# Optimization experiments

Measured on AMD Instinct MI355X. Metric: run time of the kernel, lower is better.

The kernel has to match this reference:

```python
import jax, jax.numpy as jnp
import numpy as np

B, SD, VD, AD, E, K = 32768, 96, 512, 12, 8, 2
EPS_LN = 1e-5

def _ln(x, g, b):
    m = x.mean(-1, keepdims=True)
    v = ((x - m) ** 2).mean(-1, keepdims=True)
    return (x - m) / jnp.sqrt(v + EPS_LN) * g + b

def setup_inputs() -> dict:
    key = jax.random.key(0)
    ks = iter(jax.random.split(key, 64))
    def w(shape, s=0.02):
        return jax.random.normal(next(ks), shape, dtype=jnp.float32) * s
    inp = {
        'state_obs': jax.random.normal(next(ks), (B, SD), dtype=jnp.float32),
        'vlm_feature': jax.random.normal(next(ks), (B, VD), dtype=jnp.float32),
        # state encoder (per-expert stacked): 96->256->128, Linear+ELU+LN each
        'sw1': w((E, SD, 256)), 'sb1': jnp.zeros((E, 256)), 'sg1': jnp.ones((E, 256)), 'sh1': jnp.zeros((E, 256)),
        'sw2': w((E, 256, 128)), 'sb2': jnp.zeros((E, 128)), 'sg2': jnp.ones((E, 128)), 'sh2': jnp.zeros((E, 128)),
        # vlm encoder: 512->512->256
        'vw1': w((E, VD, 512)), 'vb1': jnp.zeros((E, 512)), 'vg1': jnp.ones((E, 512)), 'vh1': jnp.zeros((E, 512)),
        'vw2': w((E, 512, 256)), 'vb2': jnp.zeros((E, 256)), 'vg2': jnp.ones((E, 256)), 'vh2': jnp.zeros((E, 256)),
        # fusion: (128+256)=384 -> 512 -> 256 -> 12 (act+LN except last)
        'fw1': w((E, 384, 512)), 'fb1': jnp.zeros((E, 512)), 'fg1': jnp.ones((E, 512)), 'fh1': jnp.zeros((E, 512)),
        'fw2': w((E, 512, 256)), 'fb2': jnp.zeros((E, 256)), 'fg2': jnp.ones((E, 256)), 'fh2': jnp.zeros((E, 256)),
        'fw3': w((E, 256, AD)), 'fb3': jnp.zeros((E, AD)),
        # gate: (96+512)=608 -> 256 -> 128 -> 8, act between hidden layers only
        'gw1': w((SD + VD, 256)), 'gb1': jnp.zeros((256,)),
        'gw2': w((256, 128)), 'gb2': jnp.zeros((128,)),
        'gw3': w((128, E)), 'gb3': jnp.zeros((E,)),
        'logstd': jnp.full((AD,), -1.0, dtype=jnp.float32),
    }
    return inp

def reference(state_obs, vlm_feature,
              sw1, sb1, sg1, sh1, sw2, sb2, sg2, sh2,
              vw1, vb1, vg1, vh1, vw2, vb2, vg2, vh2,
              fw1, fb1, fg1, fh1, fw2, fb2, fg2, fh2, fw3, fb3,
              gw1, gb1, gw2, gb2, gw3, gb3, logstd):
    act = jax.nn.elu
    # run ALL experts densely (faithful to the module)
    h = _ln(act(jnp.einsum('bi,eio->beo', state_obs, sw1) + sb1), sg1, sh1)   # [B,E,256]
    obs_feat = _ln(act(jnp.einsum('bei,eio->beo', h, sw2) + sb2), sg2, sh2)   # [B,E,128]
    h = _ln(act(jnp.einsum('bi,eio->beo', vlm_feature, vw1) + vb1), vg1, vh1) # [B,E,512]
    vlm_feat = _ln(act(jnp.einsum('bei,eio->beo', h, vw2) + vb2), vg2, vh2)   # [B,E,256]
    fused = jnp.concatenate([obs_feat, vlm_feat], axis=-1)                     # [B,E,384]
    h = _ln(act(jnp.einsum('bei,eio->beo', fused, fw1) + fb1), fg1, fh1)
    h = _ln(act(jnp.einsum('bei,eio->beo', h, fw2) + fb2), fg2, fh2)
    all_outputs = jnp.einsum('bei,eio->beo', h, fw3) + fb3                     # [B,E,AD]
    # gate
    g = jnp.concatenate([state_obs, vlm_feature], axis=-1)
    g = act(g @ gw1 + gb1)
    g = act(g @ gw2 + gb2)
    gate_logits = g @ gw3 + gb3
    gate_probs = jax.nn.softmax(gate_logits, axis=-1)                          # [B,E]
    top_k_scores, top_k_indices = jax.lax.top_k(gate_probs, K)                 # [B,K]
    selected = jnp.take_along_axis(all_outputs, top_k_indices[:, :, None], axis=1)  # [B,K,AD]
    weights = top_k_scores / (top_k_scores.sum(axis=1, keepdims=True) + 1e-9)
    fused_output = (selected * weights[:, :, None]).sum(axis=1)                # [B,AD]
    # auxiliary load-balancing loss (Switch-style)
    dispatch = jax.nn.one_hot(top_k_indices, E, dtype=gate_probs.dtype).sum(1) # [B,E]
    f = dispatch.mean(0) / K
    P = gate_probs.mean(0)
    aux_loss = E * jnp.sum(f * P)
    action = fused_output  # deterministic path
    return action, aux_loss, top_k_indices, top_k_scores
```

## Files before the change

kernel.cpp:

```cpp
#include <hip/hip_runtime.h>
#include <cstdint>
#include <cstddef>

#define BROWS 32768
#define NEXP 8
#define CAP 10240
#define CAPBLK (CAP / 64)

typedef short bf16x8 __attribute__((ext_vector_type(8)));
typedef float f32x4 __attribute__((ext_vector_type(4)));
typedef float f32x2 __attribute__((ext_vector_type(2)));

__device__ __forceinline__ unsigned short f2b(float f) {
  union { float f; unsigned u; } v; v.f = f;
  unsigned r = (v.u + 0x7fffu + ((v.u >> 16) & 1u)) >> 16;
  return (unsigned short)r;
}
__device__ __forceinline__ float b2f(unsigned short s) {
  union { unsigned u; float f; } v; v.u = ((unsigned)s) << 16; return v.f;
}
__device__ __forceinline__ float fast_elu(float x) {
  return x > 0.f ? x : __expf(x) - 1.f;
}


__global__ void k_convert_pad(const float* __restrict__ src, unsigned short* __restrict__ dst,
                              int rows, int sc, int dc) {
  int i = blockIdx.x * 256 + threadIdx.x;
  if (i >= rows * dc) return;
  int r = i / dc, c = i % dc;
  float v = (c < sc) ? src[(size_t)r * sc + c] : 0.f;
  dst[i] = f2b(v);
}

__global__ void k_wtrans(const float* __restrict__ src, unsigned short* __restrict__ dst,
                         int K, int N, int Kpad) {
  __shared__ float tile[32][33];
  int e = blockIdx.z;
  int k0 = blockIdx.x * 32, n0 = blockIdx.y * 32;
  int tx = threadIdx.x, ty = threadIdx.y;
  for (int i = 0; i < 32; i += 8) {
    int k = k0 + ty + i;
    tile[ty + i][tx] = (k < K) ? src[((size_t)e * K + k) * N + n0 + tx] : 0.f;
  }
  __syncthreads();
  for (int i = 0; i < 32; i += 8) {
    int n = n0 + ty + i;
    dst[((size_t)e * N + n) * Kpad + k0 + tx] = f2b(tile[tx][ty + i]);
  }
}

__global__ void k_zero(int* p, int n) {
  int i = blockIdx.x * 64 + threadIdx.x;
  if (i < n) p[i] = 0;
}

template<bool TWOSRC>
__launch_bounds__(256, 4)
__global__ void k_gemm32(const float* __restrict__ A0, int As0,
                         const float* __restrict__ A1, int As1, int Ks,
                         const float* __restrict__ W, const float* __restrict__ bias,
                         int K, int N, float* __restrict__ Out) {
  __shared__ float At[32][132];
  __shared__ float Bs[32][132];

  int tid = threadIdx.x;
  int rb = blockIdx.x * 128, nb = blockIdx.y * 128;
  int tx = tid & 15, tyg = tid >> 4;
  int arow = tid >> 1, aq = (tid & 1) * 16;
  int brow = tid >> 3, bc = (tid & 7) * 16;

  f32x2 acc[8][4] = {};

  float4 a0, a1, a2, a3, b0, b1, b2, b3;
  {
    const float* arp = (!TWOSRC || aq < Ks)
        ? (A0 + (size_t)(rb + arow) * As0 + aq)
        : (A1 + (size_t)(rb + arow) * As1 + (aq - Ks));
    a0 = *(const float4*)(arp);
    a1 = *(const float4*)(arp + 4);
    a2 = *(const float4*)(arp + 8);
    a3 = *(const float4*)(arp + 12);
    const float* brp = W + (size_t)brow * N + nb + bc;
    b0 = *(const float4*)(brp);
    b1 = *(const float4*)(brp + 4);
    b2 = *(const float4*)(brp + 8);
    b3 = *(const float4*)(brp + 12);
  }

  const int NT = K / 32;
  for (int kt = 0; kt < NT; ++kt) {
    __syncthreads();
    At[aq + 0][arow] = a0.x;  At[aq + 1][arow] = a0.y;
    At[aq + 2][arow] = a0.z;  At[aq + 3][arow] = a0.w;
    At[aq + 4][arow] = a1.x;  At[aq + 5][arow] = a1.y;
    At[aq + 6][arow] = a1.z;  At[aq + 7][arow] = a1.w;
    At[aq + 8][arow] = a2.x;  At[aq + 9][arow] = a2.y;
    At[aq + 10][arow] = a2.z; At[aq + 11][arow] = a2.w;
    At[aq + 12][arow] = a3.x; At[aq + 13][arow] = a3.y;
    At[aq + 14][arow] = a3.z; At[aq + 15][arow] = a3.w;
    *(float4*)(&Bs[brow][bc])      = b0;
    *(float4*)(&Bs[brow][bc + 4])  = b1;
    *(float4*)(&Bs[brow][bc + 8])  = b2;
    *(float4*)(&Bs[brow][bc + 12]) = b3;
    __syncthreads();

    if (kt + 1 < NT) {
      int ka = (kt + 1) * 32 + aq;
      const float* arp = (!TWOSRC || ka < Ks)
          ? (A0 + (size_t)(rb + arow) * As0 + ka)
          : (A1 + (size_t)(rb + arow) * As1 + (ka - Ks));
      a0 = *(const float4*)(arp);
      a1 = *(const float4*)(arp + 4);
      a2 = *(const float4*)(arp + 8);
      a3 = *(const float4*)(arp + 12);
      const float* brp = W + (size_t)((kt + 1) * 32 + brow) * N + nb + bc;
      b0 = *(const float4*)(brp);
      b1 = *(const float4*)(brp + 4);
      b2 = *(const float4*)(brp + 8);
      b3 = *(const float4*)(brp + 12);
    }

#pragma unroll 4
    for (int kk = 0; kk < 32; ++kk) {
      float4 av0 = *(const float4*)(&At[kk][tyg * 8]);
      float4 av1 = *(const float4*)(&At[kk][tyg * 8 + 4]);
      float4 bq0 = *(const float4*)(&Bs[kk][tx * 8]);
      float4 bq1 = *(const float4*)(&Bs[kk][tx * 8 + 4]);
      f32x2 bp0 = {bq0.x, bq0.y}, bp1 = {bq0.z, bq0.w};
      f32x2 bp2 = {bq1.x, bq1.y}, bp3 = {bq1.z, bq1.w};
      float av[8] = {av0.x, av0.y, av0.z, av0.w, av1.x, av1.y, av1.z, av1.w};
#pragma unroll
      for (int i = 0; i < 8; ++i) {
        f32x2 as = {av[i], av[i]};
        acc[i][0] = __builtin_elementwise_fma(as, bp0, acc[i][0]);
        acc[i][1] = __builtin_elementwise_fma(as, bp1, acc[i][1]);
        acc[i][2] = __builtin_elementwise_fma(as, bp2, acc[i][2]);
        acc[i][3] = __builtin_elementwise_fma(as, bp3, acc[i][3]);
      }
    }
  }

  float4 bia0 = *(const float4*)(&bias[nb + tx * 8]);
  float4 bia1 = *(const float4*)(&bias[nb + tx * 8 + 4]);
  float bia[8] = {bia0.x, bia0.y, bia0.z, bia0.w, bia1.x, bia1.y, bia1.z, bia1.w};

#pragma unroll
  for (int i = 0; i < 8; ++i) {
    float o[8];
#pragma unroll
    for (int j = 0; j < 4; ++j) {
      o[2 * j]     = acc[i][j][0] + bia[2 * j];
      o[2 * j + 1] = acc[i][j][1] + bia[2 * j + 1];
    }
#pragma unroll
    for (int j = 0; j < 8; ++j) o[j] = (o[j] > 0.f) ? o[j] : expm1f(o[j]);
    size_t orow = (size_t)(rb + tyg * 8 + i) * N + nb + tx * 8;
    float4 w0; w0.x = o[0]; w0.y = o[1]; w0.z = o[2]; w0.w = o[3];
    float4 w1; w1.x = o[4]; w1.y = o[5]; w1.z = o[6]; w1.w = o[7];
    *(float4*)(&Out[orow]) = w0;
    *(float4*)(&Out[orow + 4]) = w1;
  }
}

#define ACTION_SZ (32768 * 12)
#define AUX_OFF   ACTION_SZ
#define IDX_OFF   (ACTION_SZ + 1)
#define SCO_OFF   (ACTION_SZ + 1 + 32768 * 2)

__global__ void k_gatetop(const float* __restrict__ gh2,
                          const float* __restrict__ gw3, const float* __restrict__ gb3,
                          float* __restrict__ out, float* __restrict__ aux,
                          int* __restrict__ bcnt, float* __restrict__ selbuf) {
  int tid = threadIdx.x;
  int b = blockIdx.x * 256 + tid;
  int lane = tid & 63, w = tid >> 6;
  __shared__ float sprob[8];
  if (tid < 8) sprob[tid] = 0.f;
  __syncthreads();

  float lg[8];
#pragma unroll
  for (int j = 0; j < 8; ++j) lg[j] = gb3[j];
  for (int k = 0; k < 128; ++k) {
    float h = gh2[(size_t)b * 128 + k];
#pragma unroll
    for (int j = 0; j < 8; ++j) lg[j] += h * gw3[k * 8 + j];
  }
  float m = lg[0];
#pragma unroll
  for (int j = 1; j < 8; ++j) m = fmaxf(m, lg[j]);
  float probs[8], sum = 0.f;
#pragma unroll
  for (int j = 0; j < 8; ++j) { float p = expf(lg[j] - m); probs[j] = p; sum += p; }
  float inv = 1.f / sum;
#pragma unroll
  for (int j = 0; j < 8; ++j) probs[j] *= inv;
  int i0 = 0, i1;
  float v0 = -1e30f;
#pragma unroll
  for (int j = 0; j < 8; ++j) if (probs[j] > v0) { v0 = probs[j]; i0 = j; }
  float v1 = -1e30f; i1 = (i0 == 0) ? 1 : 0;
#pragma unroll
  for (int j = 0; j < 8; ++j) if (j != i0 && probs[j] > v1) { v1 = probs[j]; i1 = j; }
  float wsum = v0 + v1 + 1e-9f;
  float w0 = v0 / wsum, w1 = v1 / wsum;

  out[IDX_OFF + (size_t)b * 2 + 0] = (float)i0;
  out[IDX_OFF + (size_t)b * 2 + 1] = (float)i1;
  out[SCO_OFF + (size_t)b * 2 + 0] = v0;
  out[SCO_OFF + (size_t)b * 2 + 1] = v1;
  selbuf[(size_t)b * 4 + 0] = (float)i0;
  selbuf[(size_t)b * 4 + 1] = (float)i1;
  selbuf[(size_t)b * 4 + 2] = w0;
  selbuf[(size_t)b * 4 + 3] = w1;

#pragma unroll
  for (int e2 = 0; e2 < 8; ++e2) {
    unsigned long long mm = __ballot(i0 == e2) | __ballot(i1 == e2);
    if (lane == 0) bcnt[(blockIdx.x * 4 + w) * 8 + e2] = __popcll(mm);
  }

#pragma unroll
  for (int j = 0; j < 8; ++j) {
    float p = probs[j];
#pragma unroll
    for (int mk = 1; mk <= 32; mk <<= 1) p += __shfl_xor(p, mk, 64);
    if (lane == 0) atomicAdd(&sprob[j], p);
  }
  __syncthreads();
  if (tid < 8) atomicAdd(&aux[tid], sprob[tid]);
}

__global__ void k_scan(const int* __restrict__ bcnt, int* __restrict__ bbase,
                       int* __restrict__ cnt) {
  __shared__ int psum[8][8];
  int tid = threadIdx.x;
  int e2 = tid & 7, seg = tid >> 3;
  int s = 0;
  for (int i = 0; i < 64; ++i) s += bcnt[(seg * 64 + i) * 8 + e2];
  psum[seg][e2] = s;
  __syncthreads();
  int base = 0;
  for (int t = 0; t < seg; ++t) base += psum[t][e2];
  int run = base;
  for (int i = 0; i < 64; ++i) {
    bbase[(seg * 64 + i) * 8 + e2] = run;
    run += bcnt[(seg * 64 + i) * 8 + e2];
  }
  if (seg == 7) cnt[e2] = run;
}

__global__ void k_fill(const float* __restrict__ selbuf, const int* __restrict__ bbase,
                       int* __restrict__ perm) {
  int gidx = blockIdx.x;
  int lane = threadIdx.x;
  int b = gidx * 64 + lane;
  int i0 = (int)selbuf[(size_t)b * 4 + 0];
  int i1 = (int)selbuf[(size_t)b * 4 + 1];
  unsigned long long lt = (1ull << lane) - 1ull;
#pragma unroll
  for (int e2 = 0; e2 < 8; ++e2) {
    unsigned long long mm = __ballot(i0 == e2) | __ballot(i1 == e2);
    if (i0 == e2 || i1 == e2) {
      int s = bbase[gidx * 8 + e2] + (int)__popcll(mm & lt);
      if (s < CAP) perm[e2 * CAP + s] = b;
    }
  }
}

__global__ void k_auxfinal(const int* __restrict__ cnt, const float* __restrict__ aux,
                           float* __restrict__ out) {
  if (threadIdx.x == 0) {
    float s = 0.f;
#pragma unroll
    for (int e = 0; e < 8; ++e) {
      float f = (float)cnt[e] / (32768.f * 2.f);
      float P = aux[e] / 32768.f;
      s += f * P;
    }
    out[AUX_OFF] = 8.f * s;
  }
}

template<int K1, int N1, int N2, bool GATHER, bool FCHAIN>
__launch_bounds__(512, 4)
__global__ void k_chain(const unsigned short* __restrict__ A, int As,
                        const int* __restrict__ perm, const int* __restrict__ cnt,
                        const unsigned short* __restrict__ W1, const float* __restrict__ b1v,
                        const float* __restrict__ g1v, const float* __restrict__ h1v,
                        const unsigned short* __restrict__ W2, const float* __restrict__ b2v,
                        const float* __restrict__ g2v, const float* __restrict__ h2v,
                        unsigned short* __restrict__ Out, int Os, int Ocol,
                        const float* __restrict__ fw3, const float* __restrict__ fb3,
                        float* __restrict__ allout) {
  constexpr int WC1 = N1 / 8, NF1 = WC1 / 16;
  constexpr int WC2 = N2 / 8, NF2 = WC2 / 16;
  constexpr int NK1 = K1 / 64, NK2 = N1 / 64;
  constexpr int NS1 = NK1 * 2, NS2 = NK2 * 2;
  constexpr int PAN = (K1 > N1) ? K1 : N1;
  constexpr int NCH = N2 / 128;
  static_assert(NF1 >= 1 && NF2 >= 1 && K1 % 64 == 0 && N1 % 128 == 0, "shape");

  __shared__ unsigned short smP[64 * PAN];
  __shared__ float red[64][8][2];
  __shared__ float rowstat[64][2];

  int bid = blockIdx.x;
  int e = bid & 7;
  int count = cnt[e]; if (count > CAP) count = CAP;
  int rb = (bid >> 3) * 64;
  if (rb >= count) return;

  int tid = threadIdx.x;
  int lane = tid & 63, wn = tid >> 6;
  int l15 = lane & 15, g = lane >> 4;

  {
    int srow = tid >> 3, schunk = tid & 7;
    int slot = rb + srow;
    size_t arow;
    if (GATHER) {
      int s = slot < count ? slot : count - 1;
      arow = (size_t)perm[e * CAP + s];
    } else {
      arow = (size_t)e * CAP + slot;
    }
    const unsigned short* aptr = A + arow * As + schunk * 8;
    int lws = srow * K1 + ((schunk ^ (srow & 7)) << 3);
    uint4 stg[NK1];
#pragma unroll
    for (int kt = 0; kt < NK1; ++kt) stg[kt] = *(const uint4*)(aptr + kt * 64);
#pragma unroll
    for (int kt = 0; kt < NK1; ++kt) *(uint4*)(&smP[lws + kt * 64]) = stg[kt];
  }

  const unsigned short* W1e = W1 + (size_t)e * N1 * K1;
  const unsigned short* bp1[NF1];
#pragma unroll
  for (int nf = 0; nf < NF1; ++nf)
    bp1[nf] = W1e + (size_t)(wn * WC1 + nf * 16 + l15) * K1 + g * 8;

  f32x4 acc1[4][NF1] = {};
  bf16x8 qA[NF1], qB[NF1];
#pragma unroll
  for (int nf = 0; nf < NF1; ++nf) qA[nf] = *(const bf16x8*)(bp1[nf]);
  if (NS1 > 1) {
#pragma unroll
    for (int nf = 0; nf < NF1; ++nf) qB[nf] = *(const bf16x8*)(bp1[nf] + 32);
  }

  __syncthreads();

#pragma unroll
  for (int ks = 0; ks < NS1; ++ks) {
    const int kt = ks >> 1, kk = ks & 1;
    bf16x8 a4[4];
#pragma unroll
    for (int mf = 0; mf < 4; ++mf) {
      int row = mf * 16 + l15;
      int chunk = (kk * 4 + g) ^ (row & 7);
      a4[mf] = *(const bf16x8*)(&smP[row * K1 + kt * 64 + chunk * 8]);
    }
    if ((ks & 1) == 0) {
#pragma unroll
      for (int mf = 0; mf < 4; ++mf)
#pragma unroll
        for (int nf = 0; nf < NF1; ++nf)
          acc1[mf][nf] = __builtin_amdgcn_mfma_f32_16x16x32_bf16(a4[mf], qA[nf], acc1[mf][nf], 0, 0, 0);
      if (ks + 2 < NS1) {
#pragma unroll
        for (int nf = 0; nf < NF1; ++nf) qA[nf] = *(const bf16x8*)(bp1[nf] + (ks + 2) * 32);
      }
    } else {
#pragma unroll
      for (int mf = 0; mf < 4; ++mf)
#pragma unroll
        for (int nf = 0; nf < NF1; ++nf)
          acc1[mf][nf] = __builtin_amdgcn_mfma_f32_16x16x32_bf16(a4[mf], qB[nf], acc1[mf][nf], 0, 0, 0);
      if (ks + 2 < NS1) {
#pragma unroll
        for (int nf = 0; nf < NF1; ++nf) qB[nf] = *(const bf16x8*)(bp1[nf] + (ks + 2) * 32);
      }
    }
  }

  {
    float bia[NF1], gam[NF1], bet[NF1];
#pragma unroll
    for (int nf = 0; nf < NF1; ++nf) {
      int n = wn * WC1 + nf * 16 + l15;
      bia[nf] = b1v[e * N1 + n]; gam[nf] = g1v[e * N1 + n]; bet[nf] = h1v[e * N1 + n];
    }
#pragma unroll
    for (int mf = 0; mf < 4; ++mf)
#pragma unroll
      for (int nf = 0; nf < NF1; ++nf)
#pragma unroll
        for (int r = 0; r < 4; ++r)
          acc1[mf][nf][r] = fast_elu(acc1[mf][nf][r] + bia[nf]);
#pragma unroll
    for (int mf = 0; mf < 4; ++mf)
#pragma unroll
      for (int r = 0; r < 4; ++r) {
        float s1 = 0.f, s2 = 0.f;
#pragma unroll
        for (int nf = 0; nf < NF1; ++nf) {
          float x = acc1[mf][nf][r];
          s1 += x; s2 += x * x;
        }
#pragma unroll
        for (int mk = 1; mk <= 8; mk <<= 1) {
          s1 += __shfl_xor(s1, mk, 64);
          s2 += __shfl_xor(s2, mk, 64);
        }
        if (l15 == 0) {
          int row = mf * 16 + g * 4 + r;
          red[row][wn][0] = s1;
          red[row][wn][1] = s2;
        }
      }
    __syncthreads();
    if (tid < 64) {
      float s1 = 0.f, s2 = 0.f;
#pragma unroll
      for (int j = 0; j < 8; ++j) { s1 += red[tid][j][0]; s2 += red[tid][j][1]; }
      float mean = s1 / (float)N1;
      float var = s2 / (float)N1 - mean * mean;
      rowstat[tid][0] = mean;
      rowstat[tid][1] = rsqrtf(var + 1e-5f);
    }
    __syncthreads();
#pragma unroll
    for (int mf = 0; mf < 4; ++mf)
#pragma unroll
      for (int r = 0; r < 4; ++r) {
        int row = mf * 16 + g * 4 + r;
        float mean = rowstat[row][0], rstd = rowstat[row][1];
#pragma unroll
        for (int nf = 0; nf < NF1; ++nf) {
          int col = wn * WC1 + nf * 16 + l15;
          float y = (acc1[mf][nf][r] - mean) * rstd * gam[nf] + bet[nf];
          int pos = (col & ~63) + ((((col >> 3) & 7) ^ (row & 7)) << 3) + (col & 7);
          smP[row * N1 + pos] = f2b(y);
        }
      }
  }

  const unsigned short* W2e = W2 + (size_t)e * N2 * N1;
  const unsigned short* bp2[NF2];
#pragma unroll
  for (int nf = 0; nf < NF2; ++nf)
    bp2[nf] = W2e + (size_t)(wn * WC2 + nf * 16 + l15) * N1 + g * 8;

  f32x4 acc2[4][NF2] = {};
  bf16x8 pA[NF2], pB[NF2];
#pragma unroll
  for (int nf = 0; nf < NF2; ++nf) pA[nf] = *(const bf16x8*)(bp2[nf]);
  if (NS2 > 1) {
#pragma unroll
    for (int nf = 0; nf < NF2; ++nf) pB[nf] = *(const bf16x8*)(bp2[nf] + 32);
  }

  __syncthreads();

#pragma unroll
  for (int ks = 0; ks < NS2; ++ks) {
    const int kt = ks >> 1, kk = ks & 1;
    bf16x8 a4[4];
#pragma unroll
    for (int mf = 0; mf < 4; ++mf) {
      int row = mf * 16 + l15;
      int chunk = (kk * 4 + g) ^ (row & 7);
      a4[mf] = *(const bf16x8*)(&smP[row * N1 + kt * 64 + chunk * 8]);
    }
    if ((ks & 1) == 0) {
#pragma unroll
      for (int mf = 0; mf < 4; ++mf)
#pragma unroll
        for (int nf = 0; nf < NF2; ++nf)
          acc2[mf][nf] = __builtin_amdgcn_mfma_f32_16x16x32_bf16(a4[mf], pA[nf], acc2[mf][nf], 0, 0, 0);
      if (ks + 2 < NS2) {
#pragma unroll
        for (int nf = 0; nf < NF2; ++nf) pA[nf] = *(const bf16x8*)(bp2[nf] + (ks + 2) * 32);
      }
    } else {
#pragma unroll
      for (int mf = 0; mf < 4; ++mf)
#pragma unroll
        for (int nf = 0; nf < NF2; ++nf)
          acc2[mf][nf] = __builtin_amdgcn_mfma_f32_16x16x32_bf16(a4[mf], pB[nf], acc2[mf][nf], 0, 0, 0);
      if (ks + 2 < NS2) {
#pragma unroll
        for (int nf = 0; nf < NF2; ++nf) pB[nf] = *(const bf16x8*)(bp2[nf] + (ks + 2) * 32);
      }
    }
  }

  {
    float bia[NF2], gam[NF2], bet[NF2];
#pragma unroll
    for (int nf = 0; nf < NF2; ++nf) {
      int n = wn * WC2 + nf * 16 + l15;
      bia[nf] = b2v[e * N2 + n]; gam[nf] = g2v[e * N2 + n]; bet[nf] = h2v[e * N2 + n];
    }
#pragma unroll
    for (int mf = 0; mf < 4; ++mf)
#pragma unroll
      for (int nf = 0; nf < NF2; ++nf)
#pragma unroll
        for (int r = 0; r < 4; ++r)
          acc2[mf][nf][r] = fast_elu(acc2[mf][nf][r] + bia[nf]);
#pragma unroll
    for (int mf = 0; mf < 4; ++mf)
#pragma unroll
      for (int r = 0; r < 4; ++r) {
        float s1 = 0.f, s2 = 0.f;
#pragma unroll
        for (int nf = 0; nf < NF2; ++nf) {
          float x = acc2[mf][nf][r];
          s1 += x; s2 += x * x;
        }
#pragma unroll
        for (int mk = 1; mk <= 8; mk <<= 1) {
          s1 += __shfl_xor(s1, mk, 64);
          s2 += __shfl_xor(s2, mk, 64);
        }
        if (l15 == 0) {
          int row = mf * 16 + g * 4 + r;
          red[row][wn][0] = s1;
          red[row][wn][1] = s2;
        }
      }
    __syncthreads();
    if (tid < 64) {
      float s1 = 0.f, s2 = 0.f;
#pragma unroll
      for (int j = 0; j < 8; ++j) { s1 += red[tid][j][0]; s2 += red[tid][j][1]; }
      float mean = s1 / (float)N2;
      float var = s2 / (float)N2 - mean * mean;
      rowstat[tid][0] = mean;
      rowstat[tid][1] = rsqrtf(var + 1e-5f);
    }
    __syncthreads();
#pragma unroll
    for (int mf = 0; mf < 4; ++mf)
#pragma unroll
      for (int r = 0; r < 4; ++r) {
        int row = mf * 16 + g * 4 + r;
        float mean = rowstat[row][0], rstd = rowstat[row][1];
#pragma unroll
        for (int nf = 0; nf < NF2; ++nf)
          acc2[mf][nf][r] = (acc2[mf][nf][r] - mean) * rstd * gam[nf] + bet[nf];
      }
  }

  if constexpr (!FCHAIN) {
    unsigned short* sm16 = &smP[0];
    int wq = (wn * WC2) >> 7;
    for (int q = 0; q < NCH; ++q) {
      __syncthreads();
      if (NCH == 1 || wq == q) {
#pragma unroll
        for (int mf = 0; mf < 4; ++mf)
#pragma unroll
          for (int r = 0; r < 4; ++r) {
            int row = mf * 16 + g * 4 + r;
            int s = row & 7;
#pragma unroll
            for (int nf = 0; nf < NF2; ++nf) {
              int lc = (wn * WC2 + nf * 16 + l15) - q * 128;
              if (NCH == 1 || (lc >= 0 && lc < 128)) {
                int pos = (((lc >> 3) ^ s) << 3) | (lc & 7);
                sm16[row * 128 + pos] = f2b(acc2[mf][nf][r]);
              }
            }
          }
      }
      __syncthreads();
#pragma unroll
      for (int i = 0; i < 2; ++i) {
        int t = tid + i * 512;
        int row = t >> 4, cc = t & 15;
        int oc = cc ^ (row & 7);
        uint4 v = *(const uint4*)(&sm16[row * 128 + cc * 8]);
        *(uint4*)(&Out[((size_t)e * CAP + rb + row) * Os + Ocol + q * 128 + oc * 8]) = v;
      }
    }
  } else {
    __syncthreads();
    constexpr int H2S = 264;
    float* wsh = (float*)(&smP[64 * H2S]);
#pragma unroll
    for (int mf = 0; mf < 4; ++mf)
#pragma unroll
      for (int r = 0; r < 4; ++r) {
        int row = mf * 16 + g * 4 + r;
#pragma unroll
        for (int nf = 0; nf < NF2; ++nf) {
          int col = wn * WC2 + nf * 16 + l15;
          smP[row * H2S + col] = f2b(acc2[mf][nf][r]);
        }
      }
    for (int i = tid; i < 256 * 12; i += 512) wsh[i] = fw3[(size_t)e * 256 * 12 + i];
    __syncthreads();
#pragma unroll
    for (int it = 0; it < 2; ++it) {
      int idx = tid + it * 512;
      if (idx < 768) {
        int row = idx / 12, j = idx - row * 12;
        int slot2 = rb + row;
        if (slot2 < count) {
          float a = fb3[e * 12 + j];
          for (int c = 0; c < 256; ++c)
            a += b2f(smP[row * H2S + c]) * wsh[c * 12 + j];
          int arow = perm[e * CAP + slot2];
          allout[((size_t)arow * 8 + e) * 12 + j] = a;
        }
      }
    }
  }
}

__global__ void k_mix(const float* __restrict__ selbuf, const float* __restrict__ allout,
                      float* __restrict__ out) {
  int b = blockIdx.x * 256 + threadIdx.x;
  int i0 = (int)selbuf[(size_t)b * 4 + 0];
  int i1 = (int)selbuf[(size_t)b * 4 + 1];
  float w0 = selbuf[(size_t)b * 4 + 2];
  float w1 = selbuf[(size_t)b * 4 + 3];
  const float* a0 = allout + ((size_t)b * 8 + i0) * 12;
  const float* a1 = allout + ((size_t)b * 8 + i1) * 12;
#pragma unroll
  for (int j = 0; j < 12; ++j)
    out[(size_t)b * 12 + j] = w0 * a0[j] + w1 * a1[j];
}


extern "C" void kernel_launch(void* const* d_in, const int* in_sizes, int n_in,
                              void* d_out, int out_size, void* d_ws, size_t ws_size,
                              hipStream_t stream) {
  const float* state = (const float*)d_in[0];
  const float* vlm   = (const float*)d_in[1];
  const float* sw1 = (const float*)d_in[2];  const float* sb1 = (const float*)d_in[3];
  const float* sg1 = (const float*)d_in[4];  const float* sh1 = (const float*)d_in[5];
  const float* sw2 = (const float*)d_in[6];  const float* sb2 = (const float*)d_in[7];
  const float* sg2 = (const float*)d_in[8];  const float* sh2 = (const float*)d_in[9];
  const float* vw1 = (const float*)d_in[10]; const float* vb1 = (const float*)d_in[11];
  const float* vg1 = (const float*)d_in[12]; const float* vh1 = (const float*)d_in[13];
  const float* vw2 = (const float*)d_in[14]; const float* vb2 = (const float*)d_in[15];
  const float* vg2 = (const float*)d_in[16]; const float* vh2 = (const float*)d_in[17];
  const float* fw1 = (const float*)d_in[18]; const float* fb1 = (const float*)d_in[19];
  const float* fg1 = (const float*)d_in[20]; const float* fh1 = (const float*)d_in[21];
  const float* fw2 = (const float*)d_in[22]; const float* fb2 = (const float*)d_in[23];
  const float* fg2 = (const float*)d_in[24]; const float* fh2 = (const float*)d_in[25];
  const float* fw3 = (const float*)d_in[26]; const float* fb3 = (const float*)d_in[27];
  const float* gw1 = (const float*)d_in[28]; const float* gb1 = (const float*)d_in[29];
  const float* gw2 = (const float*)d_in[30]; const float* gb2 = (const float*)d_in[31];
  const float* gw3 = (const float*)d_in[32]; const float* gb3 = (const float*)d_in[33];

  char* ws = (char*)d_ws;
  size_t off = 0;
  auto alloc = [&](size_t bytes) -> char* {
    char* p = ws + off;
    off = (off + bytes + 255) & ~(size_t)255;
    return p;
  };
  unsigned short* st_bf = (unsigned short*)alloc((size_t)BROWS * 128 * 2);
  unsigned short* vl_bf = (unsigned short*)alloc((size_t)BROWS * 512 * 2);
  unsigned short* bufF  = (unsigned short*)alloc((size_t)NEXP * CAP * 384 * 2);
  float* allout = (float*)alloc((size_t)BROWS * 8 * 12 * 4);
  float* gh1    = (float*)alloc((size_t)BROWS * 256 * 4);
  float* gh2    = (float*)alloc((size_t)BROWS * 128 * 4);
  float* selbuf = (float*)alloc((size_t)BROWS * 4 * 4);
  int*   perm   = (int*)alloc((size_t)NEXP * CAP * 4);
  int*   bcnt   = (int*)alloc(512 * 8 * 4);
  int*   bbase  = (int*)alloc(512 * 8 * 4);
  char*  cntaux = alloc(256);
  int*   cnt = (int*)cntaux;
  float* aux = (float*)(cntaux + 64);
  unsigned short* wt_s1 = (unsigned short*)alloc((size_t)8 * 256 * 128 * 2);
  unsigned short* wt_s2 = (unsigned short*)alloc((size_t)8 * 128 * 256 * 2);
  unsigned short* wt_v1 = (unsigned short*)alloc((size_t)8 * 512 * 512 * 2);
  unsigned short* wt_v2 = (unsigned short*)alloc((size_t)8 * 256 * 512 * 2);
  unsigned short* wt_f1 = (unsigned short*)alloc((size_t)8 * 512 * 384 * 2);
  unsigned short* wt_f2 = (unsigned short*)alloc((size_t)8 * 256 * 512 * 2);
  (void)ws_size; (void)in_sizes; (void)n_in; (void)out_size;

  float* outf = (float*)d_out;

  k_convert_pad<<<(BROWS * 128 + 255) / 256, 256, 0, stream>>>(state, st_bf, BROWS, 96, 128);
  k_convert_pad<<<(BROWS * 512 + 255) / 256, 256, 0, stream>>>(vlm, vl_bf, BROWS, 512, 512);
  k_wtrans<<<dim3(4, 8, 8),   dim3(32, 8), 0, stream>>>(sw1, wt_s1, 96, 256, 128);
  k_wtrans<<<dim3(8, 4, 8),   dim3(32, 8), 0, stream>>>(sw2, wt_s2, 256, 128, 256);
  k_wtrans<<<dim3(16, 16, 8), dim3(32, 8), 0, stream>>>(vw1, wt_v1, 512, 512, 512);
  k_wtrans<<<dim3(16, 8, 8),  dim3(32, 8), 0, stream>>>(vw2, wt_v2, 512, 256, 512);
  k_wtrans<<<dim3(12, 16, 8), dim3(32, 8), 0, stream>>>(fw1, wt_f1, 384, 512, 384);
  k_wtrans<<<dim3(16, 8, 8),  dim3(32, 8), 0, stream>>>(fw2, wt_f2, 512, 256, 512);
  k_zero<<<1, 64, 0, stream>>>((int*)cntaux, 64);

  k_gemm32<true><<<dim3(256, 2), 256, 0, stream>>>(state, 96, vlm, 512, 96,
                                                   gw1, gb1, 608, 256, gh1);
  k_gemm32<false><<<dim3(256, 1), 256, 0, stream>>>(gh1, 256, nullptr, 0, 0,
                                                    gw2, gb2, 256, 128, gh2);
  k_gatetop<<<BROWS / 256, 256, 0, stream>>>(gh2, gw3, gb3, outf, aux, bcnt, selbuf);
  k_scan<<<1, 64, 0, stream>>>(bcnt, bbase, cnt);
  k_fill<<<512, 64, 0, stream>>>(selbuf, bbase, perm);
  k_auxfinal<<<1, 64, 0, stream>>>(cnt, aux, outf);

  const int NBLK = CAPBLK * NEXP;
  k_chain<128, 256, 128, true, false><<<NBLK, 512, 0, stream>>>(
      st_bf, 128, perm, cnt,
      wt_s1, sb1, sg1, sh1, wt_s2, sb2, sg2, sh2,
      bufF, 384, 0, nullptr, nullptr, nullptr);
  k_chain<512, 512, 256, true, false><<<NBLK, 512, 0, stream>>>(
      vl_bf, 512, perm, cnt,
      wt_v1, vb1, vg1, vh1, wt_v2, vb2, vg2, vh2,
      bufF, 384, 128, nullptr, nullptr, nullptr);
  k_chain<384, 512, 256, false, true><<<NBLK, 512, 0, stream>>>(
      bufF, 384, perm, cnt,
      wt_f1, fb1, fg1, fh1, wt_f2, fb2, fg2, fh2,
      nullptr, 0, 0, fw3, fb3, allout);

  k_mix<<<BROWS / 256, 256, 0, stream>>>(selbuf, allout, outf);
}
```

Before: 623.7 us.

## Merge prep, scan/aux, and state+vlm chain kernels into fewer launches

```diff
diff --git a/kernel.cpp b/kernel.cpp
--- a/kernel.cpp
+++ b/kernel.cpp
@@ -6,6 +6,7 @@
 #define NEXP 8
 #define CAP 10240
 #define CAPBLK (CAP / 64)
+#define NBLKC (CAPBLK * NEXP)
 
 typedef short bf16x8 __attribute__((ext_vector_type(8)));
 typedef float f32x4 __attribute__((ext_vector_type(4)));
@@ -23,21 +24,39 @@
   return x > 0.f ? x : __expf(x) - 1.f;
 }
 
-
-__global__ void k_convert_pad(const float* __restrict__ src, unsigned short* __restrict__ dst,
-                              int rows, int sc, int dc) {
-  int i = blockIdx.x * 256 + threadIdx.x;
-  if (i >= rows * dc) return;
-  int r = i / dc, c = i % dc;
-  float v = (c < sc) ? src[(size_t)r * sc + c] : 0.f;
-  dst[i] = f2b(v);
-}
-
-__global__ void k_wtrans(const float* __restrict__ src, unsigned short* __restrict__ dst,
-                         int K, int N, int Kpad) {
+__global__ void k_convert2(const float* __restrict__ state, const float* __restrict__ vlm,
+                           unsigned short* __restrict__ st_bf, unsigned short* __restrict__ vl_bf,
+                           int* __restrict__ cntaux) {
+  int bid = blockIdx.x, tid = threadIdx.x;
+  if (bid == 0 && tid < 64) cntaux[tid] = 0;
+  const int NB1 = (BROWS * 128) / 256;
+  if (bid < NB1) {
+    int i = bid * 256 + tid;
+    int r = i >> 7, c = i & 127;
+    st_bf[i] = f2b(c < 96 ? state[(size_t)r * 96 + c] : 0.f);
+  } else {
+    int i = (bid - NB1) * 256 + tid;
+    vl_bf[i] = f2b(vlm[i]);
+  }
+}
+
+__global__ void k_wtrans6(const float* __restrict__ s1w, unsigned short* __restrict__ s1d,
+                          const float* __restrict__ s2w, unsigned short* __restrict__ s2d,
+                          const float* __restrict__ v1w, unsigned short* __restrict__ v1d,
+                          const float* __restrict__ v2w, unsigned short* __restrict__ v2d,
+                          const float* __restrict__ f1w, unsigned short* __restrict__ f1d,
+                          const float* __restrict__ f2w, unsigned short* __restrict__ f2d) {
   __shared__ float tile[32][33];
-  int e = blockIdx.z;
-  int k0 = blockIdx.x * 32, n0 = blockIdx.y * 32;
+  int bid = blockIdx.x;
+  int e = bid / 768, r = bid % 768;
+  const float* src; unsigned short* dst; int K, N, Kpad, nbx;
+  if (r < 32)       { src = s1w; dst = s1d; K = 96;  N = 256; Kpad = 128; nbx = 4;  }
+  else if (r < 64)  { src = s2w; dst = s2d; K = 256; N = 128; Kpad = 256; nbx = 8;  r -= 32;  }
+  else if (r < 320) { src = v1w; dst = v1d; K = 512; N = 512; Kpad = 512; nbx = 16; r -= 64;  }
+  else if (r < 448) { src = v2w; dst = v2d; K = 512; N = 256; Kpad = 512; nbx = 16; r -= 320; }
+  else if (r < 640) { src = f1w; dst = f1d; K = 384; N = 512; Kpad = 384; nbx = 12; r -= 448; }
+  else              { src = f2w; dst = f2d; K = 512; N = 256; Kpad = 512; nbx = 16; r -= 640; }
+  int k0 = (r % nbx) * 32, n0 = (r / nbx) * 32;
   int tx = threadIdx.x, ty = threadIdx.y;
   for (int i = 0; i < 32; i += 8) {
     int k = k0 + ty + i;
@@ -48,11 +67,6 @@
     int n = n0 + ty + i;
     dst[((size_t)e * N + n) * Kpad + k0 + tx] = f2b(tile[tx][ty + i]);
   }
-}
-
-__global__ void k_zero(int* p, int n) {
-  int i = blockIdx.x * 64 + threadIdx.x;
-  if (i < n) p[i] = 0;
 }
 
 template<bool TWOSRC>
@@ -232,9 +246,11 @@
   if (tid < 8) atomicAdd(&aux[tid], sprob[tid]);
 }
 
-__global__ void k_scan(const int* __restrict__ bcnt, int* __restrict__ bbase,
-                       int* __restrict__ cnt) {
+__global__ void k_scanaux(const int* __restrict__ bcnt, int* __restrict__ bbase,
+                          int* __restrict__ cnt, const float* __restrict__ aux,
+                          float* __restrict__ out) {
   __shared__ int psum[8][8];
+  __shared__ int scnt[8];
   int tid = threadIdx.x;
   int e2 = tid & 7, seg = tid >> 3;
   int s = 0;
@@ -248,7 +264,15 @@
     bbase[(seg * 64 + i) * 8 + e2] = run;
     run += bcnt[(seg * 64 + i) * 8 + e2];
   }
-  if (seg == 7) cnt[e2] = run;
+  if (seg == 7) { cnt[e2] = run; scnt[e2] = run; }
+  __syncthreads();
+  if (tid == 0) {
+    float ss = 0.f;
+#pragma unroll
+    for (int e = 0; e < 8; ++e)
+      ss += ((float)scnt[e] / 65536.f) * (aux[e] / 32768.f);
+    out[AUX_OFF] = 8.f * ss;
+  }
 }
 
 __global__ void k_fill(const float* __restrict__ selbuf, const int* __restrict__ bbase,
@@ -269,44 +293,30 @@
   }
 }
 
-__global__ void k_auxfinal(const int* __restrict__ cnt, const float* __restrict__ aux,
-                           float* __restrict__ out) {
-  if (threadIdx.x == 0) {
-    float s = 0.f;
-#pragma unroll
-    for (int e = 0; e < 8; ++e) {
-      float f = (float)cnt[e] / (32768.f * 2.f);
-      float P = aux[e] / 32768.f;
-      s += f * P;
-    }
-    out[AUX_OFF] = 8.f * s;
-  }
-}
-
 template<int K1, int N1, int N2, bool GATHER, bool FCHAIN>
-__launch_bounds__(512, 4)
-__global__ void k_chain(const unsigned short* __restrict__ A, int As,
-                        const int* __restrict__ perm, const int* __restrict__ cnt,
-                        const unsigned short* __restrict__ W1, const float* __restrict__ b1v,
-                        const float* __restrict__ g1v, const float* __restrict__ h1v,
-                        const unsigned short* __restrict__ W2, const float* __restrict__ b2v,
-                        const float* __restrict__ g2v, const float* __restrict__ h2v,
-                        unsigned short* __restrict__ Out, int Os, int Ocol,
-                        const float* __restrict__ fw3, const float* __restrict__ fb3,
-                        float* __restrict__ allout) {
+__device__ __forceinline__ void chain_body(
+    int bid, char* ldsraw,
+    const unsigned short* __restrict__ A, int As,
+    const int* __restrict__ perm, const int* __restrict__ cnt,
+    const unsigned short* __restrict__ W1, const float* __restrict__ b1v,
+    const float* __restrict__ g1v, const float* __restrict__ h1v,
+    const unsigned short* __restrict__ W2, const float* __restrict__ b2v,
+    const float* __restrict__ g2v, const float* __restrict__ h2v,
+    unsigned short* __restrict__ Out, int Os, int Ocol,
+    const float* __restrict__ fw3, const float* __restrict__ fb3,
+    float* __restrict__ allout) {
   constexpr int WC1 = N1 / 8, NF1 = WC1 / 16;
   constexpr int WC2 = N2 / 8, NF2 = WC2 / 16;
-  constexpr int NK1 = K1 / 64, NK2 = N1 / 64;
-  constexpr int NS1 = NK1 * 2, NS2 = NK2 * 2;
+  constexpr int NK1 = K1 / 64;
+  constexpr int NS1 = NK1 * 2, NS2 = (N1 / 64) * 2;
   constexpr int PAN = (K1 > N1) ? K1 : N1;
   constexpr int NCH = N2 / 128;
   static_assert(NF1 >= 1 && NF2 >= 1 && K1 % 64 == 0 && N1 % 128 == 0, "shape");
 
-  __shared__ unsigned short smP[64 * PAN];
-  __shared__ float red[64][8][2];
-  __shared__ float rowstat[64][2];
-
-  int bid = blockIdx.x;
+  unsigned short* smP = (unsigned short*)ldsraw;
+  float (*red)[8][2] = (float(*)[8][2])(ldsraw + (size_t)64 * PAN * 2);
+  float (*rowstat)[2] = (float(*)[2])(ldsraw + (size_t)64 * PAN * 2 + 4096);
+
   int e = bid & 7;
   int count = cnt[e]; if (count > CAP) count = CAP;
   int rb = (bid >> 3) * 64;
@@ -620,6 +630,47 @@
       }
     }
   }
+}
+
+__launch_bounds__(512, 4)
+__global__ void k_sv(const unsigned short* __restrict__ st_bf,
+                     const unsigned short* __restrict__ vl_bf,
+                     const int* __restrict__ perm, const int* __restrict__ cnt,
+                     const unsigned short* __restrict__ wS1, const float* __restrict__ sb1,
+                     const float* __restrict__ sg1, const float* __restrict__ sh1,
+                     const unsigned short* __restrict__ wS2, const float* __restrict__ sb2,
+                     const float* __restrict__ sg2, const float* __restrict__ sh2,
+                     const unsigned short* __restrict__ wV1, const float* __restrict__ vb1,
+                     const float* __restrict__ vg1, const float* __restrict__ vh1,
+                     const unsigned short* __restrict__ wV2, const float* __restrict__ vb2,
+                     const float* __restrict__ vg2, const float* __restrict__ vh2,
+                     unsigned short* __restrict__ bufF) {
+  __shared__ char lds[70144];
+  int bid = blockIdx.x;
+  if (bid < NBLKC) {
+    chain_body<512, 512, 256, true, false>(bid, lds, vl_bf, 512, perm, cnt,
+        wV1, vb1, vg1, vh1, wV2, vb2, vg2, vh2,
+        bufF, 384, 128, nullptr, nullptr, nullptr);
+  } else {
+    chain_body<128, 256, 128, true, false>(bid - NBLKC, lds, st_bf, 128, perm, cnt,
+        wS1, sb1, sg1, sh1, wS2, sb2, sg2, sh2,
+        bufF, 384, 0, nullptr, nullptr, nullptr);
+  }
+}
+
+__launch_bounds__(512, 4)
+__global__ void k_chainF(const unsigned short* __restrict__ bufF,
+                         const int* __restrict__ perm, const int* __restrict__ cnt,
+                         const unsigned short* __restrict__ wF1, const float* __restrict__ fb1,
+                         const float* __restrict__ fg1, const float* __restrict__ fh1,
+                         const unsigned short* __restrict__ wF2, const float* __restrict__ fb2,
+                         const float* __restrict__ fg2, const float* __restrict__ fh2,
+                         const float* __restrict__ fw3, const float* __restrict__ fb3,
+                         float* __restrict__ allout) {
+  __shared__ char lds[70144];
+  chain_body<384, 512, 256, false, true>(blockIdx.x, lds, bufF, 384, perm, cnt,
+      wF1, fb1, fg1, fh1, wF2, fb2, fg2, fh2,
+      nullptr, 0, 0, fw3, fb3, allout);
 }
 
 __global__ void k_mix(const float* __restrict__ selbuf, const float* __restrict__ allout,
@@ -689,38 +740,25 @@
 
   float* outf = (float*)d_out;
 
-  k_convert_pad<<<(BROWS * 128 + 255) / 256, 256, 0, stream>>>(state, st_bf, BROWS, 96, 128);
-  k_convert_pad<<<(BROWS * 512 + 255) / 256, 256, 0, stream>>>(vlm, vl_bf, BROWS, 512, 512);
-  k_wtrans<<<dim3(4, 8, 8),   dim3(32, 8), 0, stream>>>(sw1, wt_s1, 96, 256, 128);
-  k_wtrans<<<dim3(8, 4, 8),   dim3(32, 8), 0, stream>>>(sw2, wt_s2, 256, 128, 256);
-  k_wtrans<<<dim3(16, 16, 8), dim3(32, 8), 0, stream>>>(vw1, wt_v1, 512, 512, 512);
-  k_wtrans<<<dim3(16, 8, 8),  dim3(32, 8), 0, stream>>>(vw2, wt_v2, 512, 256, 512);
-  k_wtrans<<<dim3(12, 16, 8), dim3(32, 8), 0, stream>>>(fw1, wt_f1, 384, 512, 384);
-  k_wtrans<<<dim3(16, 8, 8),  dim3(32, 8), 0, stream>>>(fw2, wt_f2, 512, 256, 512);
-  k_zero<<<1, 64, 0, stream>>>((int*)cntaux, 64);
+  const int NBCV = (BROWS * 128) / 256 + (BROWS * 512) / 256;
+  k_convert2<<<NBCV, 256, 0, stream>>>(state, vlm, st_bf, vl_bf, (int*)cntaux);
+  k_wtrans6<<<768 * 8, dim3(32, 8), 0, stream>>>(sw1, wt_s1, sw2, wt_s2,
+                                                 vw1, wt_v1, vw2, wt_v2,
+                                                 fw1, wt_f1, fw2, wt_f2);
 
   k_gemm32<true><<<dim3(256, 2), 256, 0, stream>>>(state, 96, vlm, 512, 96,
                                                    gw1, gb1, 608, 256, gh1);
   k_gemm32<false><<<dim3(256, 1), 256, 0, stream>>>(gh1, 256, nullptr, 0, 0,
                                                     gw2, gb2, 256, 128, gh2);
   k_gatetop<<<BROWS / 256, 256, 0, stream>>>(gh2, gw3, gb3, outf, aux, bcnt, selbuf);
-  k_scan<<<1, 64, 0, stream>>>(bcnt, bbase, cnt);
+  k_scanaux<<<1, 64, 0, stream>>>(bcnt, bbase, cnt, aux, outf);
   k_fill<<<512, 64, 0, stream>>>(selbuf, bbase, perm);
-  k_auxfinal<<<1, 64, 0, stream>>>(cnt, aux, outf);
-
-  const int NBLK = CAPBLK * NEXP;
-  k_chain<128, 256, 128, true, false><<<NBLK, 512, 0, stream>>>(
-      st_bf, 128, perm, cnt,
+
+  k_sv<<<2 * NBLKC, 512, 0, stream>>>(st_bf, vl_bf, perm, cnt,
       wt_s1, sb1, sg1, sh1, wt_s2, sb2, sg2, sh2,
-      bufF, 384, 0, nullptr, nullptr, nullptr);
-  k_chain<512, 512, 256, true, false><<<NBLK, 512, 0, stream>>>(
-      vl_bf, 512, perm, cnt,
-      wt_v1, vb1, vg1, vh1, wt_v2, vb2, vg2, vh2,
-      bufF, 384, 128, nullptr, nullptr, nullptr);
-  k_chain<384, 512, 256, false, true><<<NBLK, 512, 0, stream>>>(
-      bufF, 384, perm, cnt,
-      wt_f1, fb1, fg1, fh1, wt_f2, fb2, fg2, fh2,
-      nullptr, 0, 0, fw3, fb3, allout);
+      wt_v1, vb1, vg1, vh1, wt_v2, vb2, vg2, vh2, bufF);
+  k_chainF<<<NBLKC, 512, 0, stream>>>(bufF, perm, cnt,
+      wt_f1, fb1, fg1, fh1, wt_f2, fb2, fg2, fh2, fw3, fb3, allout);
 
   k_mix<<<BROWS / 256, 256, 0, stream>>>(selbuf, allout, outf);
 }
```

New measurement: 588.0 us. 1.06x faster.
